# Kernel tuning notes

Hardware: AMD Instinct MI355X
Metric: run time of the kernel (lower is better)

## Reference

```python
import jax, jax.numpy as jnp
import numpy as np

H = 16          # head_count
D = 1024        # model_dim
DPH = D // H    # dim_per_head


def setup_inputs() -> dict:
    key0 = jax.random.key(0)
    ks = jax.random.split(key0, 13)
    B, S = 4, 2048
    scale = 1.0 / np.sqrt(D)
    inp = {
        "key": jax.random.normal(ks[0], (B, S, D), jnp.float32),
        "value": jax.random.normal(ks[1], (B, S, D), jnp.float32),
        "query": jax.random.normal(ks[2], (B, S, D), jnp.float32),
        "mask": jax.random.randint(ks[3], (B, S, S), 0, 2).astype(jnp.bool_),
        "Wq": jax.random.normal(ks[4], (D, D), jnp.float32) * scale,
        "bq": jnp.zeros((D,), jnp.float32),
        "Wk": jax.random.normal(ks[5], (D, D), jnp.float32) * scale,
        "bk": jnp.zeros((D,), jnp.float32),
        "Wv": jax.random.normal(ks[6], (D, D), jnp.float32) * scale,
        "bv": jnp.zeros((D,), jnp.float32),
        "Wo": jax.random.normal(ks[7], (D, D), jnp.float32) * scale,
        "bo": jnp.zeros((D,), jnp.float32),
    }
    return inp


def _shape(x, B):
    # [B, S, D] -> [B, H, S, DPH]
    return x.reshape(B, -1, H, DPH).transpose(0, 2, 1, 3)


def reference(key, value, query, mask, Wq, bq, Wk, bk, Wv, bv, Wo, bo):
    B, S, _ = key.shape
    k_up = _shape(key @ Wk + bk, B)                       # [B,H,S,DPH]
    v_up = _shape(value @ Wv + bv, B)                     # [B,H,S,DPH]
    q_up = _shape(query @ Wq + bq, B) / jnp.sqrt(jnp.asarray(DPH, key.dtype))
    scores = jnp.einsum('bhqd,bhkd->bhqk', q_up, k_up)    # [B,H,S,S]
    scores = jnp.where(mask[:, None, :, :], jnp.asarray(-1e18, scores.dtype), scores)
    attn = jax.nn.softmax(scores, axis=-1)                # dropout = identity (eval)
    context = jnp.einsum('bhqk,bhkd->bhqd', attn, v_up)   # [B,H,S,DPH]
    context = context.transpose(0, 2, 1, 3).reshape(B, S, H * DPH)
    return context @ Wo + bo
```

## Files before the change

### kernel.cpp

```cpp
#include <hip/hip_runtime.h>

typedef _Float16 half8 __attribute__((ext_vector_type(8)));
typedef _Float16 half4 __attribute__((ext_vector_type(4)));
typedef float floatx4 __attribute__((ext_vector_type(4)));
typedef float floatx16 __attribute__((ext_vector_type(16)));

#define MFMA16(A,B,C) __builtin_amdgcn_mfma_f32_16x16x32_f16((A),(B),(C),0,0,0)
#define MFMA32(A,B,C) __builtin_amdgcn_mfma_f32_32x32x16_f16((A),(B),(C),0,0,0)


__global__ __launch_bounds__(256) void maskpack(
    const int* __restrict__ m, unsigned int* __restrict__ p)
{
  const int w = blockIdx.x * 256 + threadIdx.x;
  const int b = w >> 17;
  const int rem = w & 131071;
  const int s = rem >> 6;
  const int wp = rem & 63;
  const int4* src = (const int4*)(m + (size_t)w * 32);
  unsigned int bits = 0;
#pragma unroll
  for (int j = 0; j < 8; ++j) {
    const int4 v = src[j];
    bits |= (v.x ? 1u : 0u) << (j * 4 + 0);
    bits |= (v.y ? 1u : 0u) << (j * 4 + 1);
    bits |= (v.z ? 1u : 0u) << (j * 4 + 2);
    bits |= (v.w ? 1u : 0u) << (j * 4 + 3);
  }
  p[((size_t)(b * 64 + wp)) * 2048 + s] = bits;
}

__global__ __launch_bounds__(256) void wconv(
    const float* __restrict__ Wq, const float* __restrict__ Wk,
    const float* __restrict__ Wv, const float* __restrict__ Wo,
    _Float16* __restrict__ dst)
{
  const float* W = (blockIdx.z == 0) ? Wq : (blockIdx.z == 1) ? Wk
                  : (blockIdx.z == 2) ? Wv : Wo;
  _Float16* WT = dst + (size_t)blockIdx.z * 1024 * 1024;
  __shared__ float t[32][33];
  const int tx = threadIdx.x & 31;
  const int ty = threadIdx.x >> 5;
  const int k0 = blockIdx.x * 32, n0 = blockIdx.y * 32;
#pragma unroll
  for (int j = 0; j < 4; ++j)
    t[ty + j * 8][tx] = W[(size_t)(k0 + ty + j * 8) * 1024 + n0 + tx];
  __syncthreads();
#pragma unroll
  for (int j = 0; j < 4; ++j)
    WT[(size_t)(n0 + ty + j * 8) * 1024 + k0 + tx] = (_Float16)t[tx][ty + j * 8];
}

template <int OP>
__global__ __launch_bounds__(256) void gemm_k(
    const void* __restrict__ Ap, const _Float16* __restrict__ BT,
    const float* __restrict__ bias, void* __restrict__ Cp)
{
  __shared__ __align__(16) _Float16 As[128 * 64];
  __shared__ __align__(16) _Float16 Bs[128 * 64];
  const int tid = threadIdx.x;
  const int lane = tid & 63;
  const int wv = tid >> 6;
  const int m0 = blockIdx.x * 128;
  const int n0 = blockIdx.y * 128;
  const int wr = (wv >> 1) * 64;
  const int wc = (wv & 1) * 64;

  floatx4 acc[4][4];
#pragma unroll
  for (int i = 0; i < 4; ++i)
#pragma unroll
    for (int j = 0; j < 4; ++j) acc[i][j] = (floatx4){0.f, 0.f, 0.f, 0.f};

  char* AsB = (char*)As;
  char* BsB = (char*)Bs;

  for (int ko = 0; ko < 1024; ko += 64) {
#pragma unroll
    for (int r = 0; r < 4; ++r) {
      const int idx = (r * 256 + tid) * 8;
      const int row = idx >> 6;
      const int colh = idx & 63;
      const int dstb = row * 128 + ((colh * 2) ^ ((row & 7) << 4));
      if (OP == 3) {
        const _Float16* s = (const _Float16*)Ap + (size_t)(m0 + row) * 1024 + ko + colh;
        *(half8*)(AsB + dstb) = *(const half8*)s;
      } else {
        const float* s = (const float*)Ap + (size_t)(m0 + row) * 1024 + ko + colh;
        floatx4 v0 = *(const floatx4*)s;
        floatx4 v1 = *(const floatx4*)(s + 4);
        union { half8 v; unsigned int u[4]; } pk;
        pk.u[0] = __builtin_bit_cast(unsigned int, __builtin_amdgcn_cvt_pkrtz(v0[0], v0[1]));
        pk.u[1] = __builtin_bit_cast(unsigned int, __builtin_amdgcn_cvt_pkrtz(v0[2], v0[3]));
        pk.u[2] = __builtin_bit_cast(unsigned int, __builtin_amdgcn_cvt_pkrtz(v1[0], v1[1]));
        pk.u[3] = __builtin_bit_cast(unsigned int, __builtin_amdgcn_cvt_pkrtz(v1[2], v1[3]));
        *(half8*)(AsB + dstb) = pk.v;
      }
      const _Float16* bs = BT + (size_t)(n0 + row) * 1024 + ko + colh;
      *(half8*)(BsB + dstb) = *(const half8*)bs;
    }
    __syncthreads();
#pragma unroll
    for (int kk = 0; kk < 64; kk += 32) {
      half8 af[4], bf[4];
#pragma unroll
      for (int mi = 0; mi < 4; ++mi) {
        const int row = wr + mi * 16 + (lane & 15);
        const int cb = (kk + (lane >> 4) * 8) * 2;
        af[mi] = *(const half8*)(AsB + row * 128 + (cb ^ ((row & 7) << 4)));
      }
#pragma unroll
      for (int ni = 0; ni < 4; ++ni) {
        const int row = wc + ni * 16 + (lane & 15);
        const int cb = (kk + (lane >> 4) * 8) * 2;
        bf[ni] = *(const half8*)(BsB + row * 128 + (cb ^ ((row & 7) << 4)));
      }
#pragma unroll
      for (int mi = 0; mi < 4; ++mi)
#pragma unroll
        for (int ni = 0; ni < 4; ++ni)
          acc[mi][ni] = MFMA16(af[mi], bf[ni], acc[mi][ni]);
    }
    __syncthreads();
  }

#pragma unroll
  for (int ni = 0; ni < 4; ++ni) {
    const int nn = n0 + wc + ni * 16 + (lane & 15);
    const float bvv = bias[nn];
#pragma unroll
    for (int mi = 0; mi < 4; ++mi) {
      floatx4 c = acc[mi][ni];
#pragma unroll
      for (int i = 0; i < 4; ++i) {
        const int mm = m0 + wr + mi * 16 + (lane >> 4) * 4 + i;
        float val = c[i] + bvv;
        if (OP == 0) val *= 0.1803368801111204f;
        if (OP == 0 || OP == 1) {
          _Float16* o = (_Float16*)Cp;
          const size_t off =
              ((size_t)((mm >> 11) * 16 + (nn >> 6)) * 2048 + (mm & 2047)) * 64 + (nn & 63);
          o[off] = (_Float16)val;
        } else if (OP == 2) {
          _Float16* o = (_Float16*)Cp;
          const int mmp = (mm & ~0xC) | ((mm & 4) << 1) | ((mm & 8) >> 1);
          const size_t off =
              ((size_t)((mm >> 11) * 16 + (nn >> 6)) * 64 + (nn & 63)) * 2048 + (mmp & 2047);
          o[off] = (_Float16)val;
        } else {
          float* o = (float*)Cp;
          o[(size_t)mm * 1024 + nn] = val;
        }
      }
    }
  }
}

__global__ __launch_bounds__(256) void attn_k(
    const _Float16* __restrict__ q_up, const _Float16* __restrict__ k_up,
    const _Float16* __restrict__ vT, const unsigned int* __restrict__ pmaskT,
    _Float16* __restrict__ ctx)
{
  const int tid = threadIdx.x;
  const int lane = tid & 63;
  const int wv = tid >> 6;
  const int bid = blockIdx.x;
  const int xcd = bid & 7;
  const int slot = bid >> 3;
  const int bh = xcd * 8 + (slot & 7);
  const int qc = slot >> 3;
  const int b = bh >> 4;
  const int h = bh & 15;
  const int l31 = lane & 31;
  const int hi = lane >> 5;
  const int qw = qc * 256 + wv * 64;

  __shared__ __align__(16) _Float16 Kl[2][32 * 64];
  __shared__ __align__(16) _Float16 Vl[2][64 * 32];

  const _Float16* qb = q_up + ((size_t)bh * 2048 + qw) * 64;
  const _Float16* kb = k_up + (size_t)bh * 2048 * 64;
  const _Float16* vb = vT + (size_t)bh * 64 * 2048;
  const unsigned int* mbase = pmaskT + (size_t)(b * 64) * 2048 + qw + l31;

  const int krow = tid >> 3, kseg = tid & 7;
  const int kByte = krow * 128 + ((kseg * 16) ^ ((krow & 7) << 4));
  const int vrow = tid >> 2, vseg = tid & 3;
  const int vByte = vrow * 64 + ((vseg * 16) ^ (((vrow >> 1) & 3) << 4));
  const _Float16* gK = kb + tid * 8;
  const _Float16* gV = vb + (size_t)vrow * 2048 + vseg * 8;
  char* KB = (char*)Kl;
  char* VB = (char*)Vl;

  half8 qf[2][4];
#pragma unroll
  for (int qt = 0; qt < 2; ++qt)
#pragma unroll
    for (int kk = 0; kk < 4; ++kk)
      qf[qt][kk] = *(const half8*)(qb + (size_t)(qt * 32 + l31) * 64 + kk * 16 + hi * 8);

  floatx16 O[2][2];
#pragma unroll
  for (int qt = 0; qt < 2; ++qt)
#pragma unroll
    for (int dt = 0; dt < 2; ++dt)
#pragma unroll
      for (int r = 0; r < 16; ++r) O[qt][dt][r] = 0.f;
  float lsum[2] = {0.f, 0.f};

  floatx16 zero16;
#pragma unroll
  for (int r = 0; r < 16; ++r) zero16[r] = 0.f;

  half8 stK, stV;

  auto COMPUTE = [&](int buf, int t) {
    unsigned int mw[2];
    mw[0] = mbase[(size_t)t * 2048];
    mw[1] = mbase[(size_t)t * 2048 + 32];
    half8 kf[4];
#pragma unroll
    for (int kk = 0; kk < 4; ++kk)
      kf[kk] = *(const half8*)(KB + buf * 4096 + l31 * 128 +
                               ((kk * 32 + hi * 16) ^ ((l31 & 7) << 4)));
    half8 vf[2][2];
#pragma unroll
    for (int dt = 0; dt < 2; ++dt)
#pragma unroll
      for (int kk2 = 0; kk2 < 2; ++kk2)
        vf[dt][kk2] = *(const half8*)(VB + buf * 4096 + (dt * 32 + l31) * 64 +
                                      ((kk2 * 32 + hi * 16) ^ (((l31 >> 1) & 3) << 4)));

    floatx16 s[2];
    __builtin_amdgcn_s_setprio(1);
#pragma unroll
    for (int qt = 0; qt < 2; ++qt) {
      floatx16 a;
      a = MFMA32(kf[0], qf[qt][0], zero16);
      a = MFMA32(kf[1], qf[qt][1], a);
      a = MFMA32(kf[2], qf[qt][2], a);
      s[qt] = MFMA32(kf[3], qf[qt][3], a);
    }
    __builtin_amdgcn_s_setprio(0);

#pragma unroll
    for (int qt = 0; qt < 2; ++qt) {
      const unsigned int mh = mw[qt] >> (4 * hi);
      float e[16];
#pragma unroll
      for (int m = 0; m < 4; ++m) {
        const unsigned int bm = mh >> (8 * m);
#pragma unroll
        for (int j = 0; j < 4; ++j)
          e[4 * m + j] =
              ((bm >> j) & 1u) ? 0.f : __builtin_amdgcn_exp2f(s[qt][4 * m + j]);
      }
      float u0 = (e[0] + e[1]) + (e[2] + e[3]);
      float u1 = (e[4] + e[5]) + (e[6] + e[7]);
      float u2 = (e[8] + e[9]) + (e[10] + e[11]);
      float u3 = (e[12] + e[13]) + (e[14] + e[15]);
      lsum[qt] += (u0 + u1) + (u2 + u3);

      union { half8 v; unsigned int u[4]; } p0, p1;
      p0.u[0] = __builtin_bit_cast(unsigned int, __builtin_amdgcn_cvt_pkrtz(e[0], e[1]));
      p0.u[1] = __builtin_bit_cast(unsigned int, __builtin_amdgcn_cvt_pkrtz(e[2], e[3]));
      p0.u[2] = __builtin_bit_cast(unsigned int, __builtin_amdgcn_cvt_pkrtz(e[4], e[5]));
      p0.u[3] = __builtin_bit_cast(unsigned int, __builtin_amdgcn_cvt_pkrtz(e[6], e[7]));
      p1.u[0] = __builtin_bit_cast(unsigned int, __builtin_amdgcn_cvt_pkrtz(e[8], e[9]));
      p1.u[1] = __builtin_bit_cast(unsigned int, __builtin_amdgcn_cvt_pkrtz(e[10], e[11]));
      p1.u[2] = __builtin_bit_cast(unsigned int, __builtin_amdgcn_cvt_pkrtz(e[12], e[13]));
      p1.u[3] = __builtin_bit_cast(unsigned int, __builtin_amdgcn_cvt_pkrtz(e[14], e[15]));
      __builtin_amdgcn_s_setprio(1);
#pragma unroll
      for (int dt = 0; dt < 2; ++dt) {
        O[qt][dt] = MFMA32(vf[dt][0], p0.v, O[qt][dt]);
        O[qt][dt] = MFMA32(vf[dt][1], p1.v, O[qt][dt]);
      }
      __builtin_amdgcn_s_setprio(0);
    }
  };

  stK = *(const half8*)gK;
  stV = *(const half8*)gV;
  *(half8*)(KB + kByte) = stK;
  *(half8*)(VB + vByte) = stV;
  stK = *(const half8*)(gK + 2048);
  stV = *(const half8*)(gV + 32);
  __syncthreads();

#pragma unroll 1
  for (int t = 0; t < 64; t += 2) {
    {
      *(half8*)(KB + 4096 + kByte) = stK;
      *(half8*)(VB + 4096 + vByte) = stV;
      const int tn = (t + 2 < 64) ? t + 2 : 0;
      stK = *(const half8*)(gK + (size_t)tn * 2048);
      stV = *(const half8*)(gV + tn * 32);
      COMPUTE(0, t);
      __syncthreads();
    }
    {
      *(half8*)(KB + kByte) = stK;
      *(half8*)(VB + vByte) = stV;
      const int tn = (t + 3 < 64) ? t + 3 : 0;
      stK = *(const half8*)(gK + (size_t)tn * 2048);
      stV = *(const half8*)(gV + tn * 32);
      COMPUTE(1, t + 1);
      __syncthreads();
    }
  }

#pragma unroll
  for (int qt = 0; qt < 2; ++qt) {
    const float tot = lsum[qt] + __shfl_xor(lsum[qt], 32);
    const float inv = 1.f / tot;
    const size_t rowb = ((size_t)(b * 2048 + qw + qt * 32 + l31)) * 1024 + h * 64;
#pragma unroll
    for (int dt = 0; dt < 2; ++dt) {
#pragma unroll
      for (int m = 0; m < 4; ++m) {
        half4 w4;
        w4[0] = (_Float16)(O[qt][dt][4 * m + 0] * inv);
        w4[1] = (_Float16)(O[qt][dt][4 * m + 1] * inv);
        w4[2] = (_Float16)(O[qt][dt][4 * m + 2] * inv);
        w4[3] = (_Float16)(O[qt][dt][4 * m + 3] * inv);
        *(half4*)(ctx + rowb + dt * 32 + 8 * m + 4 * hi) = w4;
      }
    }
  }
}

extern "C" void kernel_launch(void* const* d_in, const int* in_sizes, int n_in,
                              void* d_out, int out_size, void* d_ws, size_t ws_size,
                              hipStream_t stream) {
  const float* key   = (const float*)d_in[0];
  const float* value = (const float*)d_in[1];
  const float* query = (const float*)d_in[2];
  const int*   mask  = (const int*)d_in[3];
  const float* Wq = (const float*)d_in[4];
  const float* bq = (const float*)d_in[5];
  const float* Wk = (const float*)d_in[6];
  const float* bk = (const float*)d_in[7];
  const float* Wv = (const float*)d_in[8];
  const float* bv = (const float*)d_in[9];
  const float* Wo = (const float*)d_in[10];
  const float* bo = (const float*)d_in[11];

  _Float16* wsp = (_Float16*)d_ws;
  _Float16* WT   = wsp;
  _Float16* q_up = wsp + (size_t)4 * 1024 * 1024;
  _Float16* k_up = q_up + (size_t)8192 * 1024;
  _Float16* vT   = k_up + (size_t)8192 * 1024;
  _Float16* ctx  = vT + (size_t)8192 * 1024;
  unsigned int* pmaskT = (unsigned int*)(ctx + (size_t)8192 * 1024);

  maskpack<<<dim3(2048), 256, 0, stream>>>(mask, pmaskT);
  wconv<<<dim3(32, 32, 4), 256, 0, stream>>>(Wq, Wk, Wv, Wo, WT);
  gemm_k<0><<<dim3(64, 8), 256, 0, stream>>>(query, WT, bq, q_up);
  gemm_k<1><<<dim3(64, 8), 256, 0, stream>>>(key, WT + (size_t)1024 * 1024, bk, k_up);
  gemm_k<2><<<dim3(64, 8), 256, 0, stream>>>(value, WT + (size_t)2 * 1024 * 1024, bv, vT);
  attn_k<<<dim3(512), 256, 0, stream>>>(q_up, k_up, vT, pmaskT, ctx);
  gemm_k<3><<<dim3(64, 8), 256, 0, stream>>>(ctx, WT + (size_t)3 * 1024 * 1024, bo, (float*)d_out);
}
```

Measured before the change: 276.2 us.

## Pre-convert activations to fp16, use direct global-to-LDS loads, stage GEMM epilogues through LDS

Adds an aconv kernel that converts each fp32 activation tensor to fp16 in a scratch buffer (reusing ctx) before its projection GEMM. This lets the GEMM fill shared memory with global_load_lds direct copies using an XOR-swizzled layout. All GEMM epilogues now stage results in shared memory and write coalesced 16-byte vectors for the head-split, transposed-V and fp32 output layouts, replacing scattered 2- and 4-byte stores. The cost is three extra conversion passes over 32MB fp32 inputs, plus extra barriers in the epilogue.

```diff
diff --git a/kernel.cpp b/kernel.cpp
--- a/kernel.cpp
+++ b/kernel.cpp
@@ -7,6 +7,11 @@
 
 #define MFMA16(A,B,C) __builtin_amdgcn_mfma_f32_16x16x32_f16((A),(B),(C),0,0,0)
 #define MFMA32(A,B,C) __builtin_amdgcn_mfma_f32_32x32x16_f16((A),(B),(C),0,0,0)
+
+#define GLOAD_LDS(G, L)                                                        \
+  __builtin_amdgcn_global_load_lds(                                            \
+      (const __attribute__((address_space(1))) unsigned int*)(G),              \
+      (__attribute__((address_space(3))) unsigned int*)(L), 16, 0, 0)
 
 
 __global__ __launch_bounds__(256) void maskpack(
@@ -51,13 +56,28 @@
     WT[(size_t)(n0 + ty + j * 8) * 1024 + k0 + tx] = (_Float16)t[tx][ty + j * 8];
 }
 
+__global__ __launch_bounds__(256) void aconv(
+    const float* __restrict__ s, _Float16* __restrict__ d)
+{
+  const size_t i = ((size_t)blockIdx.x * 256 + threadIdx.x) * 8;
+  floatx4 v0 = *(const floatx4*)(s + i);
+  floatx4 v1 = *(const floatx4*)(s + i + 4);
+  union { half8 v; unsigned int u[4]; } pk;
+  pk.u[0] = __builtin_bit_cast(unsigned int, __builtin_amdgcn_cvt_pkrtz(v0[0], v0[1]));
+  pk.u[1] = __builtin_bit_cast(unsigned int, __builtin_amdgcn_cvt_pkrtz(v0[2], v0[3]));
+  pk.u[2] = __builtin_bit_cast(unsigned int, __builtin_amdgcn_cvt_pkrtz(v1[0], v1[1]));
+  pk.u[3] = __builtin_bit_cast(unsigned int, __builtin_amdgcn_cvt_pkrtz(v1[2], v1[3]));
+  *(half8*)(d + i) = pk.v;
+}
+
 template <int OP>
 __global__ __launch_bounds__(256) void gemm_k(
-    const void* __restrict__ Ap, const _Float16* __restrict__ BT,
+    const _Float16* __restrict__ Ah, const _Float16* __restrict__ BT,
     const float* __restrict__ bias, void* __restrict__ Cp)
 {
-  __shared__ __align__(16) _Float16 As[128 * 64];
-  __shared__ __align__(16) _Float16 Bs[128 * 64];
+  __shared__ __align__(16) char smem[32768];
+  char* AsB = smem;
+  char* BsB = smem + 16384;
   const int tid = threadIdx.x;
   const int lane = tid & 63;
   const int wv = tid >> 6;
@@ -72,32 +92,16 @@
 #pragma unroll
     for (int j = 0; j < 4; ++j) acc[i][j] = (floatx4){0.f, 0.f, 0.f, 0.f};
 
-  char* AsB = (char*)As;
-  char* BsB = (char*)Bs;
+  const int grow = lane >> 3;
+  const int gslot = (lane & 7) ^ grow;
 
   for (int ko = 0; ko < 1024; ko += 64) {
 #pragma unroll
-    for (int r = 0; r < 4; ++r) {
-      const int idx = (r * 256 + tid) * 8;
-      const int row = idx >> 6;
-      const int colh = idx & 63;
-      const int dstb = row * 128 + ((colh * 2) ^ ((row & 7) << 4));
-      if (OP == 3) {
-        const _Float16* s = (const _Float16*)Ap + (size_t)(m0 + row) * 1024 + ko + colh;
-        *(half8*)(AsB + dstb) = *(const half8*)s;
-      } else {
-        const float* s = (const float*)Ap + (size_t)(m0 + row) * 1024 + ko + colh;
-        floatx4 v0 = *(const floatx4*)s;
-        floatx4 v1 = *(const floatx4*)(s + 4);
-        union { half8 v; unsigned int u[4]; } pk;
-        pk.u[0] = __builtin_bit_cast(unsigned int, __builtin_amdgcn_cvt_pkrtz(v0[0], v0[1]));
-        pk.u[1] = __builtin_bit_cast(unsigned int, __builtin_amdgcn_cvt_pkrtz(v0[2], v0[3]));
-        pk.u[2] = __builtin_bit_cast(unsigned int, __builtin_amdgcn_cvt_pkrtz(v1[0], v1[1]));
-        pk.u[3] = __builtin_bit_cast(unsigned int, __builtin_amdgcn_cvt_pkrtz(v1[2], v1[3]));
-        *(half8*)(AsB + dstb) = pk.v;
-      }
-      const _Float16* bs = BT + (size_t)(n0 + row) * 1024 + ko + colh;
-      *(half8*)(BsB + dstb) = *(const half8*)bs;
+    for (int it = 0; it < 4; ++it) {
+      const int c = wv * 4 + it;
+      const int row = c * 8 + grow;
+      GLOAD_LDS(Ah + (size_t)(m0 + row) * 1024 + ko + gslot * 8, AsB + c * 1024);
+      GLOAD_LDS(BT + (size_t)(n0 + row) * 1024 + ko + gslot * 8, BsB + c * 1024);
     }
     __syncthreads();
 #pragma unroll
@@ -124,33 +128,93 @@
     __syncthreads();
   }
 
-#pragma unroll
-  for (int ni = 0; ni < 4; ++ni) {
-    const int nn = n0 + wc + ni * 16 + (lane & 15);
-    const float bvv = bias[nn];
-#pragma unroll
-    for (int mi = 0; mi < 4; ++mi) {
-      floatx4 c = acc[mi][ni];
-#pragma unroll
-      for (int i = 0; i < 4; ++i) {
-        const int mm = m0 + wr + mi * 16 + (lane >> 4) * 4 + i;
-        float val = c[i] + bvv;
-        if (OP == 0) val *= 0.1803368801111204f;
-        if (OP == 0 || OP == 1) {
-          _Float16* o = (_Float16*)Cp;
-          const size_t off =
-              ((size_t)((mm >> 11) * 16 + (nn >> 6)) * 2048 + (mm & 2047)) * 64 + (nn & 63);
-          o[off] = (_Float16)val;
-        } else if (OP == 2) {
-          _Float16* o = (_Float16*)Cp;
-          const int mmp = (mm & ~0xC) | ((mm & 4) << 1) | ((mm & 8) >> 1);
-          const size_t off =
-              ((size_t)((mm >> 11) * 16 + (nn >> 6)) * 64 + (nn & 63)) * 2048 + (mmp & 2047);
-          o[off] = (_Float16)val;
-        } else {
-          float* o = (float*)Cp;
-          o[(size_t)mm * 1024 + nn] = val;
+  if (OP == 0 || OP == 1) {
+#pragma unroll
+    for (int ni = 0; ni < 4; ++ni) {
+      const int nloc = wc + ni * 16 + (lane & 15);
+      const float bvv = bias[n0 + nloc];
+#pragma unroll
+      for (int mi = 0; mi < 4; ++mi) {
+        floatx4 c = acc[mi][ni];
+        const int mb = wr + mi * 16 + (lane >> 4) * 4;
+#pragma unroll
+        for (int i = 0; i < 4; ++i) {
+          float val = c[i] + bvv;
+          if (OP == 0) val *= 0.1803368801111204f;
+          ((_Float16*)smem)[(mb + i) * 128 + nloc] = (_Float16)val;
         }
+      }
+    }
+    __syncthreads();
+    const int mloc = tid & 127, hseg = tid >> 7;
+    const int batch = m0 >> 11;
+    const int head = (n0 >> 6) + hseg;
+    _Float16* dst = (_Float16*)Cp +
+        (((size_t)(batch * 16 + head)) * 2048 + (m0 & 2047) + mloc) * 64;
+    const _Float16* srcr = (const _Float16*)smem + mloc * 128 + hseg * 64;
+#pragma unroll
+    for (int c8 = 0; c8 < 8; ++c8) {
+      const int cc = (c8 + (tid & 7)) & 7;
+      *(half8*)(dst + cc * 8) = *(const half8*)(srcr + cc * 8);
+    }
+  } else if (OP == 2) {
+#pragma unroll
+    for (int ni = 0; ni < 4; ++ni) {
+      const int nloc = wc + ni * 16 + (lane & 15);
+      const float bvv = bias[n0 + nloc];
+#pragma unroll
+      for (int mi = 0; mi < 4; ++mi) {
+        floatx4 c = acc[mi][ni];
+        const int mb = wr + mi * 16 + (lane >> 4) * 4;
+        const int mp = (mb & ~0xC) | ((mb & 4) << 1) | ((mb & 8) >> 1);
+        half4 w4;
+        w4[0] = (_Float16)(c[0] + bvv);
+        w4[1] = (_Float16)(c[1] + bvv);
+        w4[2] = (_Float16)(c[2] + bvv);
+        w4[3] = (_Float16)(c[3] + bvv);
+        *(half4*)((_Float16*)smem + nloc * 128 + mp) = w4;
+      }
+    }
+    __syncthreads();
+    const int rn = tid & 127, sh = tid >> 7;
+    const int batch = m0 >> 11;
+    const int head = (n0 >> 6) + (rn >> 6);
+    const int d = rn & 63;
+    _Float16* dst = (_Float16*)Cp +
+        (((size_t)(batch * 16 + head)) * 64 + d) * 2048 + (m0 & 2047) + sh * 64;
+    const _Float16* srcr = (const _Float16*)smem + rn * 128 + sh * 64;
+#pragma unroll
+    for (int c8 = 0; c8 < 8; ++c8) {
+      const int cc = (c8 + (tid & 7)) & 7;
+      *(half8*)(dst + cc * 8) = *(const half8*)(srcr + cc * 8);
+    }
+  } else {
+#pragma unroll 1
+    for (int nh = 0; nh < 2; ++nh) {
+      __syncthreads();
+      if (wc == nh * 64) {
+#pragma unroll
+        for (int ni = 0; ni < 4; ++ni) {
+          const int nl = ni * 16 + (lane & 15);
+          const float bvv = bias[n0 + nh * 64 + nl];
+#pragma unroll
+          for (int mi = 0; mi < 4; ++mi) {
+            floatx4 c = acc[mi][ni];
+            const int mb = wr + mi * 16 + (lane >> 4) * 4;
+#pragma unroll
+            for (int i = 0; i < 4; ++i)
+              ((float*)smem)[(mb + i) * 64 + nl] = c[i] + bvv;
+          }
+        }
+      }
+      __syncthreads();
+      const int mloc = tid & 127, h2 = tid >> 7;
+      float* dst = (float*)Cp + (size_t)(m0 + mloc) * 1024 + n0 + nh * 64 + h2 * 32;
+      const float* srcr = (const float*)smem + mloc * 64 + h2 * 32;
+#pragma unroll
+      for (int c4 = 0; c4 < 8; ++c4) {
+        const int cc = (c4 + (tid & 7)) & 7;
+        *(floatx4*)(dst + cc * 4) = *(const floatx4*)(srcr + cc * 4);
       }
     }
   }
@@ -353,12 +417,16 @@
   _Float16* vT   = k_up + (size_t)8192 * 1024;
   _Float16* ctx  = vT + (size_t)8192 * 1024;
   unsigned int* pmaskT = (unsigned int*)(ctx + (size_t)8192 * 1024);
+  _Float16* ascr = ctx;
 
   maskpack<<<dim3(2048), 256, 0, stream>>>(mask, pmaskT);
   wconv<<<dim3(32, 32, 4), 256, 0, stream>>>(Wq, Wk, Wv, Wo, WT);
-  gemm_k<0><<<dim3(64, 8), 256, 0, stream>>>(query, WT, bq, q_up);
-  gemm_k<1><<<dim3(64, 8), 256, 0, stream>>>(key, WT + (size_t)1024 * 1024, bk, k_up);
-  gemm_k<2><<<dim3(64, 8), 256, 0, stream>>>(value, WT + (size_t)2 * 1024 * 1024, bv, vT);
+  aconv<<<dim3(4096), 256, 0, stream>>>(query, ascr);
+  gemm_k<0><<<dim3(64, 8), 256, 0, stream>>>(ascr, WT, bq, q_up);
+  aconv<<<dim3(4096), 256, 0, stream>>>(key, ascr);
+  gemm_k<1><<<dim3(64, 8), 256, 0, stream>>>(ascr, WT + (size_t)1024 * 1024, bk, k_up);
+  aconv<<<dim3(4096), 256, 0, stream>>>(value, ascr);
+  gemm_k<2><<<dim3(64, 8), 256, 0, stream>>>(ascr, WT + (size_t)2 * 1024 * 1024, bv, vT);
   attn_k<<<dim3(512), 256, 0, stream>>>(q_up, k_up, vT, pmaskT, ctx);
   gemm_k<3><<<dim3(64, 8), 256, 0, stream>>>(ctx, WT + (size_t)3 * 1024 * 1024, bo, (float*)d_out);
 }
```

Result: slower. 301.2 us (+9.0%).

## Split attention block into 8 waves of 32 query rows each

Applied to the files above, without the earlier changes.

The attention kernel goes from 4 waves handling 64 query rows each to 8 waves handling 32 rows each, launched with 512 threads per block. The K/V staging is split so the first 256 threads load K and the rest load V, one vector each per tile. The aim is more waves per CU to hide latency, with fewer registers per wave. In exchange, each K/V tile loaded into LDS is reused across fewer rows per wave, and the 8 waves pay more barrier synchronisation.

```diff
diff --git a/kernel.cpp b/kernel.cpp
--- a/kernel.cpp
+++ b/kernel.cpp
@@ -156,7 +156,7 @@
   }
 }
 
-__global__ __launch_bounds__(256) void attn_k(
+__global__ __launch_bounds__(512) void attn_k(
     const _Float16* __restrict__ q_up, const _Float16* __restrict__ k_up,
     const _Float16* __restrict__ vT, const unsigned int* __restrict__ pmaskT,
     _Float16* __restrict__ ctx)
@@ -173,7 +173,7 @@
   const int h = bh & 15;
   const int l31 = lane & 31;
   const int hi = lane >> 5;
-  const int qw = qc * 256 + wv * 64;
+  const int qw = qc * 256 + wv * 32;
 
   __shared__ __align__(16) _Float16 Kl[2][32 * 64];
   __shared__ __align__(16) _Float16 Vl[2][64 * 32];
@@ -183,41 +183,39 @@
   const _Float16* vb = vT + (size_t)bh * 64 * 2048;
   const unsigned int* mbase = pmaskT + (size_t)(b * 64) * 2048 + qw + l31;
 
-  const int krow = tid >> 3, kseg = tid & 7;
-  const int kByte = krow * 128 + ((kseg * 16) ^ ((krow & 7) << 4));
-  const int vrow = tid >> 2, vseg = tid & 3;
-  const int vByte = vrow * 64 + ((vseg * 16) ^ (((vrow >> 1) & 3) << 4));
-  const _Float16* gK = kb + tid * 8;
-  const _Float16* gV = vb + (size_t)vrow * 2048 + vseg * 8;
+  const bool isK = tid < 256;
+  const int st = isK ? tid : tid - 256;
+  const int krow = st >> 3, kseg = st & 7;
+  const int vrow = st >> 2, vseg = st & 3;
+  const int sOff = isK ? (krow * 128 + ((kseg * 16) ^ ((krow & 7) << 4)))
+                       : (vrow * 64 + ((vseg * 16) ^ (((vrow >> 1) & 3) << 4)));
+  const _Float16* gsrc = isK ? (kb + (size_t)st * 8)
+                             : (vb + (size_t)vrow * 2048 + vseg * 8);
+  const int gstride = isK ? 2048 : 32;
+  char* Lbase = isK ? (char*)Kl : (char*)Vl;
   char* KB = (char*)Kl;
   char* VB = (char*)Vl;
 
-  half8 qf[2][4];
-#pragma unroll
-  for (int qt = 0; qt < 2; ++qt)
-#pragma unroll
-    for (int kk = 0; kk < 4; ++kk)
-      qf[qt][kk] = *(const half8*)(qb + (size_t)(qt * 32 + l31) * 64 + kk * 16 + hi * 8);
-
-  floatx16 O[2][2];
-#pragma unroll
-  for (int qt = 0; qt < 2; ++qt)
-#pragma unroll
-    for (int dt = 0; dt < 2; ++dt)
-#pragma unroll
-      for (int r = 0; r < 16; ++r) O[qt][dt][r] = 0.f;
-  float lsum[2] = {0.f, 0.f};
+  half8 qf[4];
+#pragma unroll
+  for (int kk = 0; kk < 4; ++kk)
+    qf[kk] = *(const half8*)(qb + (size_t)l31 * 64 + kk * 16 + hi * 8);
+
+  floatx16 O[2];
+#pragma unroll
+  for (int dt = 0; dt < 2; ++dt)
+#pragma unroll
+    for (int r = 0; r < 16; ++r) O[dt][r] = 0.f;
+  float lsum = 0.f;
 
   floatx16 zero16;
 #pragma unroll
   for (int r = 0; r < 16; ++r) zero16[r] = 0.f;
 
-  half8 stK, stV;
+  half8 stg;
 
   auto COMPUTE = [&](int buf, int t) {
-    unsigned int mw[2];
-    mw[0] = mbase[(size_t)t * 2048];
-    mw[1] = mbase[(size_t)t * 2048 + 32];
+    const unsigned int mw = mbase[(size_t)t * 2048];
     half8 kf[4];
 #pragma unroll
     for (int kk = 0; kk < 4; ++kk)
@@ -231,99 +229,86 @@
         vf[dt][kk2] = *(const half8*)(VB + buf * 4096 + (dt * 32 + l31) * 64 +
                                       ((kk2 * 32 + hi * 16) ^ (((l31 >> 1) & 3) << 4)));
 
-    floatx16 s[2];
+    floatx16 s;
     __builtin_amdgcn_s_setprio(1);
-#pragma unroll
-    for (int qt = 0; qt < 2; ++qt) {
+    {
       floatx16 a;
-      a = MFMA32(kf[0], qf[qt][0], zero16);
-      a = MFMA32(kf[1], qf[qt][1], a);
-      a = MFMA32(kf[2], qf[qt][2], a);
-      s[qt] = MFMA32(kf[3], qf[qt][3], a);
+      a = MFMA32(kf[0], qf[0], zero16);
+      a = MFMA32(kf[1], qf[1], a);
+      a = MFMA32(kf[2], qf[2], a);
+      s = MFMA32(kf[3], qf[3], a);
     }
     __builtin_amdgcn_s_setprio(0);
 
-#pragma unroll
-    for (int qt = 0; qt < 2; ++qt) {
-      const unsigned int mh = mw[qt] >> (4 * hi);
-      float e[16];
-#pragma unroll
-      for (int m = 0; m < 4; ++m) {
-        const unsigned int bm = mh >> (8 * m);
-#pragma unroll
-        for (int j = 0; j < 4; ++j)
-          e[4 * m + j] =
-              ((bm >> j) & 1u) ? 0.f : __builtin_amdgcn_exp2f(s[qt][4 * m + j]);
-      }
-      float u0 = (e[0] + e[1]) + (e[2] + e[3]);
-      float u1 = (e[4] + e[5]) + (e[6] + e[7]);
-      float u2 = (e[8] + e[9]) + (e[10] + e[11]);
-      float u3 = (e[12] + e[13]) + (e[14] + e[15]);
-      lsum[qt] += (u0 + u1) + (u2 + u3);
-
-      union { half8 v; unsigned int u[4]; } p0, p1;
-      p0.u[0] = __builtin_bit_cast(unsigned int, __builtin_amdgcn_cvt_pkrtz(e[0], e[1]));
-      p0.u[1] = __builtin_bit_cast(unsigned int, __builtin_amdgcn_cvt_pkrtz(e[2], e[3]));
-      p0.u[2] = __builtin_bit_cast(unsigned int, __builtin_amdgcn_cvt_pkrtz(e[4], e[5]));
-      p0.u[3] = __builtin_bit_cast(unsigned int, __builtin_amdgcn_cvt_pkrtz(e[6], e[7]));
-      p1.u[0] = __builtin_bit_cast(unsigned int, __builtin_amdgcn_cvt_pkrtz(e[8], e[9]));
-      p1.u[1] = __builtin_bit_cast(unsigned int, __builtin_amdgcn_cvt_pkrtz(e[10], e[11]));
-      p1.u[2] = __builtin_bit_cast(unsigned int, __builtin_amdgcn_cvt_pkrtz(e[12], e[13]));
-      p1.u[3] = __builtin_bit_cast(unsigned int, __builtin_amdgcn_cvt_pkrtz(e[14], e[15]));
-      __builtin_amdgcn_s_setprio(1);
-#pragma unroll
-      for (int dt = 0; dt < 2; ++dt) {
-        O[qt][dt] = MFMA32(vf[dt][0], p0.v, O[qt][dt]);
-        O[qt][dt] = MFMA32(vf[dt][1], p1.v, O[qt][dt]);
-      }
-      __builtin_amdgcn_s_setprio(0);
-    }
+    const unsigned int mh = mw >> (4 * hi);
+    float e[16];
+#pragma unroll
+    for (int m = 0; m < 4; ++m) {
+      const unsigned int bm = mh >> (8 * m);
+#pragma unroll
+      for (int j = 0; j < 4; ++j)
+        e[4 * m + j] = ((bm >> j) & 1u) ? 0.f : __builtin_amdgcn_exp2f(s[4 * m + j]);
+    }
+    float u0 = (e[0] + e[1]) + (e[2] + e[3]);
+    float u1 = (e[4] + e[5]) + (e[6] + e[7]);
+    float u2 = (e[8] + e[9]) + (e[10] + e[11]);
+    float u3 = (e[12] + e[13]) + (e[14] + e[15]);
+    lsum += (u0 + u1) + (u2 + u3);
+
+    union { half8 v; unsigned int u[4]; } p0, p1;
+    p0.u[0] = __builtin_bit_cast(unsigned int, __builtin_amdgcn_cvt_pkrtz(e[0], e[1]));
+    p0.u[1] = __builtin_bit_cast(unsigned int, __builtin_amdgcn_cvt_pkrtz(e[2], e[3]));
+    p0.u[2] = __builtin_bit_cast(unsigned int, __builtin_amdgcn_cvt_pkrtz(e[4], e[5]));
+    p0.u[3] = __builtin_bit_cast(unsigned int, __builtin_amdgcn_cvt_pkrtz(e[6], e[7]));
+    p1.u[0] = __builtin_bit_cast(unsigned int, __builtin_amdgcn_cvt_pkrtz(e[8], e[9]));
+    p1.u[1] = __builtin_bit_cast(unsigned int, __builtin_amdgcn_cvt_pkrtz(e[10], e[11]));
+    p1.u[2] = __builtin_bit_cast(unsigned int, __builtin_amdgcn_cvt_pkrtz(e[12], e[13]));
+    p1.u[3] = __builtin_bit_cast(unsigned int, __builtin_amdgcn_cvt_pkrtz(e[14], e[15]));
+    __builtin_amdgcn_s_setprio(1);
+#pragma unroll
+    for (int dt = 0; dt < 2; ++dt) {
+      O[dt] = MFMA32(vf[dt][0], p0.v, O[dt]);
+      O[dt] = MFMA32(vf[dt][1], p1.v, O[dt]);
+    }
+    __builtin_amdgcn_s_setprio(0);
   };
 
-  stK = *(const half8*)gK;
-  stV = *(const half8*)gV;
-  *(half8*)(KB + kByte) = stK;
-  *(half8*)(VB + vByte) = stV;
-  stK = *(const half8*)(gK + 2048);
-  stV = *(const half8*)(gV + 32);
+  stg = *(const half8*)gsrc;
+  *(half8*)(Lbase + sOff) = stg;
+  stg = *(const half8*)(gsrc + gstride);
   __syncthreads();
 
 #pragma unroll 1
   for (int t = 0; t < 64; t += 2) {
     {
-      *(half8*)(KB + 4096 + kByte) = stK;
-      *(half8*)(VB + 4096 + vByte) = stV;
+      *(half8*)(Lbase + 4096 + sOff) = stg;
       const int tn = (t + 2 < 64) ? t + 2 : 0;
-      stK = *(const half8*)(gK + (size_t)tn * 2048);
-      stV = *(const half8*)(gV + tn * 32);
+      stg = *(const half8*)(gsrc + (size_t)tn * gstride);
       COMPUTE(0, t);
       __syncthreads();
     }
     {
-      *(half8*)(KB + kByte) = stK;
-      *(half8*)(VB + vByte) = stV;
+      *(half8*)(Lbase + sOff) = stg;
       const int tn = (t + 3 < 64) ? t + 3 : 0;
-      stK = *(const half8*)(gK + (size_t)tn * 2048);
-      stV = *(const half8*)(gV + tn * 32);
+      stg = *(const half8*)(gsrc + (size_t)tn * gstride);
       COMPUTE(1, t + 1);
       __syncthreads();
     }
   }
 
-#pragma unroll
-  for (int qt = 0; qt < 2; ++qt) {
-    const float tot = lsum[qt] + __shfl_xor(lsum[qt], 32);
+  {
+    const float tot = lsum + __shfl_xor(lsum, 32);
     const float inv = 1.f / tot;
-    const size_t rowb = ((size_t)(b * 2048 + qw + qt * 32 + l31)) * 1024 + h * 64;
+    const size_t rowb = ((size_t)(b * 2048 + qw + l31)) * 1024 + h * 64;
 #pragma unroll
     for (int dt = 0; dt < 2; ++dt) {
 #pragma unroll
       for (int m = 0; m < 4; ++m) {
         half4 w4;
-        w4[0] = (_Float16)(O[qt][dt][4 * m + 0] * inv);
-        w4[1] = (_Float16)(O[qt][dt][4 * m + 1] * inv);
-        w4[2] = (_Float16)(O[qt][dt][4 * m + 2] * inv);
-        w4[3] = (_Float16)(O[qt][dt][4 * m + 3] * inv);
+        w4[0] = (_Float16)(O[dt][4 * m + 0] * inv);
+        w4[1] = (_Float16)(O[dt][4 * m + 1] * inv);
+        w4[2] = (_Float16)(O[dt][4 * m + 2] * inv);
+        w4[3] = (_Float16)(O[dt][4 * m + 3] * inv);
         *(half4*)(ctx + rowb + dt * 32 + 8 * m + 4 * hi) = w4;
       }
     }
@@ -359,6 +344,6 @@
   gemm_k<0><<<dim3(64, 8), 256, 0, stream>>>(query, WT, bq, q_up);
   gemm_k<1><<<dim3(64, 8), 256, 0, stream>>>(key, WT + (size_t)1024 * 1024, bk, k_up);
   gemm_k<2><<<dim3(64, 8), 256, 0, stream>>>(value, WT + (size_t)2 * 1024 * 1024, bv, vT);
-  attn_k<<<dim3(512), 256, 0, stream>>>(q_up, k_up, vT, pmaskT, ctx);
+  attn_k<<<dim3(512), 512, 0, stream>>>(q_up, k_up, vT, pmaskT, ctx);
   gemm_k<3><<<dim3(64, 8), 256, 0, stream>>>(ctx, WT + (size_t)3 * 1024 * 1024, bo, (float*)d_out);
 }
```

Measured after the change: 253.3 us (median of 2 runs). 8.3% less time.
